# Optimization experiments

Hardware: AMD Instinct MI355X
Metric: run time of the kernel (lower is better)

The kernel has to match this reference:

```python
import jax, jax.numpy as jnp
import numpy as np

D_MODEL = 768
NUM_HEADS = 12
D_K = D_MODEL // NUM_HEADS


def setup_inputs() -> dict:
    key = jax.random.key(0)
    ks = jax.random.split(key, 11)
    B, S = 4, 2048
    s = 1.0 / np.sqrt(D_MODEL)
    return {
        "query": jax.random.normal(ks[0], (B, S, D_MODEL), jnp.float32),
        "key": jax.random.normal(ks[1], (B, S, D_MODEL), jnp.float32),
        "value": jax.random.normal(ks[2], (B, S, D_MODEL), jnp.float32),
        "Wq": jax.random.normal(ks[3], (D_MODEL, D_MODEL), jnp.float32) * s,
        "bq": jnp.zeros((D_MODEL,), jnp.float32),
        "Wk": jax.random.normal(ks[4], (D_MODEL, D_MODEL), jnp.float32) * s,
        "bk": jnp.zeros((D_MODEL,), jnp.float32),
        "Wv": jax.random.normal(ks[5], (D_MODEL, D_MODEL), jnp.float32) * s,
        "bv": jnp.zeros((D_MODEL,), jnp.float32),
        "Wo": jax.random.normal(ks[6], (D_MODEL, D_MODEL), jnp.float32) * s,
        "bo": jnp.zeros((D_MODEL,), jnp.float32),
    }


def reference(query, key, value, Wq, bq, Wk, bk, Wv, bv, Wo, bo):
    B, S, _ = query.shape

    def split_heads(x):  # [B,S,D] -> [B,H,S,dk]
        return x.reshape(B, -1, NUM_HEADS, D_K).transpose(0, 2, 1, 3)

    Q = split_heads(query @ Wq + bq)
    K = split_heads(key @ Wk + bk)
    V = split_heads(value @ Wv + bv)

    scale = 1.0 / jnp.sqrt(jnp.asarray(D_K, Q.dtype))
    scores = jnp.einsum("bhqd,bhkd->bhqk", Q, K) * scale  # [B,H,S,S]
    attn_weights = jax.nn.softmax(scores, axis=-1)
    attn_out = jnp.einsum("bhqk,bhkd->bhqd", attn_weights, V)

    out = attn_out.transpose(0, 2, 1, 3).reshape(B, -1, D_MODEL)
    out = out @ Wo + bo
    return (out, attn_weights)
```

## Files before the change

kernel.cpp:

```cpp
#include <hip/hip_runtime.h>


#define D_MODEL 768
#define NH 12
#define DK 64
#define BATCH 4
#define SEQ 2048
#define BS (BATCH * SEQ)
#define HEADS_TOTAL (BATCH * NH)

__global__ __launch_bounds__(256)
void gemm_bias_kernel(const float* __restrict__ A, const float* __restrict__ W,
                      const float* __restrict__ bias, float* __restrict__ C,
                      int M, int N, int K, int remap)
{
    __shared__ float As[16][136];
    __shared__ float Bs[16][136];
    const int t  = threadIdx.x;
    const int tx = t & 15, ty = t >> 4;
    const int m0 = blockIdx.y * 128;
    const int n0 = blockIdx.x * 128;

    float acc[8][8];
#pragma unroll
    for (int i = 0; i < 8; ++i)
#pragma unroll
        for (int j = 0; j < 8; ++j) acc[i][j] = 0.f;

    for (int kt = 0; kt < K; kt += 16) {
#pragma unroll
        for (int i = 0; i < 2; ++i) {
            int L = t + i * 256;
            int m = L >> 2, kq = (L & 3) * 4;
            float4 v = *(const float4*)(A + (size_t)(m0 + m) * K + kt + kq);
            As[kq + 0][m] = v.x; As[kq + 1][m] = v.y;
            As[kq + 2][m] = v.z; As[kq + 3][m] = v.w;
        }
#pragma unroll
        for (int i = 0; i < 2; ++i) {
            int L = t + i * 256;
            int kk = L >> 5, nq = (L & 31) * 4;
            *(float4*)&Bs[kk][nq] = *(const float4*)(W + (size_t)(kt + kk) * N + n0 + nq);
        }
        __syncthreads();
#pragma unroll
        for (int kk = 0; kk < 16; ++kk) {
            float a[8], b[8];
            *(float4*)&a[0] = *(float4*)&As[kk][ty * 8];
            *(float4*)&a[4] = *(float4*)&As[kk][ty * 8 + 4];
            *(float4*)&b[0] = *(float4*)&Bs[kk][tx * 8];
            *(float4*)&b[4] = *(float4*)&Bs[kk][tx * 8 + 4];
#pragma unroll
            for (int i = 0; i < 8; ++i)
#pragma unroll
                for (int j = 0; j < 8; ++j)
                    acc[i][j] += a[i] * b[j];
        }
        __syncthreads();
    }

    float bv[8];
    *(float4*)&bv[0] = *(const float4*)(bias + n0 + tx * 8);
    *(float4*)&bv[4] = *(const float4*)(bias + n0 + tx * 8 + 4);

#pragma unroll
    for (int i = 0; i < 8; ++i) {
        int m = m0 + ty * 8 + i;
        float o[8];
#pragma unroll
        for (int j = 0; j < 8; ++j) o[j] = acc[i][j] + bv[j];
        float* dst;
        if (remap) {
            int n = n0 + tx * 8;
            int b = m >> 11, s = m & 2047, h = n >> 6, d = n & 63;
            dst = C + (((size_t)(b * NH + h)) << 17) + ((size_t)s << 6) + d;
        } else {
            dst = C + (size_t)m * N + n0 + tx * 8;
        }
        *(float4*)dst       = make_float4(o[0], o[1], o[2], o[3]);
        *(float4*)(dst + 4) = make_float4(o[4], o[5], o[6], o[7]);
    }
}

__global__ __launch_bounds__(256)
void qkv_gemm_kernel(const float* __restrict__ Aq, const float* __restrict__ Ak,
                     const float* __restrict__ Av,
                     const float* __restrict__ Wq, const float* __restrict__ Wk,
                     const float* __restrict__ Wv,
                     const float* __restrict__ bq, const float* __restrict__ bk,
                     const float* __restrict__ bv,
                     float* __restrict__ Cq, float* __restrict__ Ck,
                     float* __restrict__ Cv)
{
    const float* A; const float* W; const float* bias; float* C;
    if (blockIdx.z == 0)      { A = Aq; W = Wq; bias = bq; C = Cq; }
    else if (blockIdx.z == 1) { A = Ak; W = Wk; bias = bk; C = Ck; }
    else                      { A = Av; W = Wv; bias = bv; C = Cv; }

    __shared__ float As[16][136];
    __shared__ float Bs[16][136];
    const int t  = threadIdx.x;
    const int tx = t & 15, ty = t >> 4;
    const int m0 = blockIdx.y * 128;
    const int n0 = blockIdx.x * 128;

    float acc[8][8];
#pragma unroll
    for (int i = 0; i < 8; ++i)
#pragma unroll
        for (int j = 0; j < 8; ++j) acc[i][j] = 0.f;

    for (int kt = 0; kt < D_MODEL; kt += 16) {
#pragma unroll
        for (int i = 0; i < 2; ++i) {
            int L = t + i * 256;
            int m = L >> 2, kq = (L & 3) * 4;
            float4 v = *(const float4*)(A + (size_t)(m0 + m) * D_MODEL + kt + kq);
            As[kq + 0][m] = v.x; As[kq + 1][m] = v.y;
            As[kq + 2][m] = v.z; As[kq + 3][m] = v.w;
        }
#pragma unroll
        for (int i = 0; i < 2; ++i) {
            int L = t + i * 256;
            int kk = L >> 5, nq = (L & 31) * 4;
            *(float4*)&Bs[kk][nq] = *(const float4*)(W + (size_t)(kt + kk) * D_MODEL + n0 + nq);
        }
        __syncthreads();
#pragma unroll
        for (int kk = 0; kk < 16; ++kk) {
            float a[8], b[8];
            *(float4*)&a[0] = *(float4*)&As[kk][ty * 8];
            *(float4*)&a[4] = *(float4*)&As[kk][ty * 8 + 4];
            *(float4*)&b[0] = *(float4*)&Bs[kk][tx * 8];
            *(float4*)&b[4] = *(float4*)&Bs[kk][tx * 8 + 4];
#pragma unroll
            for (int i = 0; i < 8; ++i)
#pragma unroll
                for (int j = 0; j < 8; ++j)
                    acc[i][j] += a[i] * b[j];
        }
        __syncthreads();
    }

    float bvv[8];
    *(float4*)&bvv[0] = *(const float4*)(bias + n0 + tx * 8);
    *(float4*)&bvv[4] = *(const float4*)(bias + n0 + tx * 8 + 4);

#pragma unroll
    for (int i = 0; i < 8; ++i) {
        int m = m0 + ty * 8 + i;
        float o[8];
#pragma unroll
        for (int j = 0; j < 8; ++j) o[j] = acc[i][j] + bvv[j];
        int n = n0 + tx * 8;
        int b = m >> 11, s = m & 2047, h = n >> 6, d = n & 63;
        float* dst = C + (((size_t)(b * NH + h)) << 17) + ((size_t)s << 6) + d;
        *(float4*)dst       = make_float4(o[0], o[1], o[2], o[3]);
        *(float4*)(dst + 4) = make_float4(o[4], o[5], o[6], o[7]);
    }
}

__global__ __launch_bounds__(256)
void scores_kernel(const float* __restrict__ Qh, const float* __restrict__ Kh,
                   float* __restrict__ attn, float* __restrict__ rowsum)
{
    __shared__ float Qs[32][132];
    __shared__ float Ks[32][132];
    const int t  = threadIdx.x;
    const int tx = t & 15, ty = t >> 4;
    const int bh = blockIdx.z;
    const int q0 = blockIdx.y * 128;
    const int n0 = blockIdx.x * 128;
    const float* Q  = Qh + ((size_t)bh << 17);
    const float* Kp = Kh + ((size_t)bh << 17);
    float* attnBH   = attn + ((size_t)bh << 22);

    float acc[8][8];
#pragma unroll
    for (int i = 0; i < 8; ++i)
#pragma unroll
        for (int j = 0; j < 8; ++j) acc[i][j] = 0.f;

    for (int kt = 0; kt < DK; kt += 32) {
#pragma unroll
        for (int i = 0; i < 4; ++i) {
            int L = t + i * 256;
            int r = L >> 3, c4 = (L & 7) * 4;
            float4 v = *(const float4*)(Q  + (size_t)(q0 + r) * DK + kt + c4);
            Qs[c4 + 0][r] = v.x; Qs[c4 + 1][r] = v.y;
            Qs[c4 + 2][r] = v.z; Qs[c4 + 3][r] = v.w;
            float4 w = *(const float4*)(Kp + (size_t)(n0 + r) * DK + kt + c4);
            Ks[c4 + 0][r] = w.x; Ks[c4 + 1][r] = w.y;
            Ks[c4 + 2][r] = w.z; Ks[c4 + 3][r] = w.w;
        }
        __syncthreads();
#pragma unroll
        for (int kk = 0; kk < 32; ++kk) {
            float a[8], b[8];
            *(float4*)&a[0] = *(float4*)&Qs[kk][ty * 8];
            *(float4*)&a[4] = *(float4*)&Qs[kk][ty * 8 + 4];
            *(float4*)&b[0] = *(float4*)&Ks[kk][tx * 8];
            *(float4*)&b[4] = *(float4*)&Ks[kk][tx * 8 + 4];
#pragma unroll
            for (int i = 0; i < 8; ++i)
#pragma unroll
                for (int j = 0; j < 8; ++j)
                    acc[i][j] += a[i] * b[j];
        }
        __syncthreads();
    }

    float rs[8];
#pragma unroll
    for (int i = 0; i < 8; ++i) {
        float r = 0.f;
#pragma unroll
        for (int j = 0; j < 8; ++j) {
            float e = __expf(acc[i][j] * 0.125f);
            acc[i][j] = e;
            r += e;
        }
        rs[i] = r;
        float* dst = attnBH + (size_t)(q0 + ty * 8 + i) * SEQ + n0 + tx * 8;
        *(float4*)dst       = make_float4(acc[i][0], acc[i][1], acc[i][2], acc[i][3]);
        *(float4*)(dst + 4) = make_float4(acc[i][4], acc[i][5], acc[i][6], acc[i][7]);
    }
#pragma unroll
    for (int i = 0; i < 8; ++i) {
        float r = rs[i];
        r += __shfl_xor(r, 1, 16);
        r += __shfl_xor(r, 2, 16);
        r += __shfl_xor(r, 4, 16);
        r += __shfl_xor(r, 8, 16);
        if (tx == 0)
            atomicAdd(rowsum + (size_t)bh * SEQ + q0 + ty * 8 + i, r);
    }
}

__global__ __launch_bounds__(256)
void av_kernel(const float* __restrict__ Vh, float* __restrict__ attn,
               const float* __restrict__ rowsum, float* __restrict__ AO)
{
    __shared__ float es[64][36];
    __shared__ float Vs[32][68];
    __shared__ float rsl[64];
    const int t  = threadIdx.x;
    const int tx = t & 15, ty = t >> 4;
    const int bh = blockIdx.y;
    const int q0 = blockIdx.x * 64;
    const float* V = Vh + ((size_t)bh << 17);
    float* attnBH  = attn + ((size_t)bh << 22);

    if (t < 64) rsl[t] = 1.0f / rowsum[(size_t)bh * SEQ + q0 + t];

    const int er = t >> 3,  ec = (t & 7) * 4;
    const int vr = t >> 4,  vc = (t & 15) * 4;

    float* gA0 = attnBH + (size_t)(q0 + er) * SEQ + ec;
    float* gA1 = attnBH + (size_t)(q0 + er + 32) * SEQ + ec;
    const float* gV0 = V + (size_t)vr * DK + vc;
    const float* gV1 = gV0 + 16 * DK;

    float4 pe0 = *(const float4*)gA0;
    float4 pe1 = *(const float4*)gA1;
    float4 pv0 = *(const float4*)gV0;
    float4 pv1 = *(const float4*)gV1;

    float acc[4][4];
#pragma unroll
    for (int i = 0; i < 4; ++i)
#pragma unroll
        for (int j = 0; j < 4; ++j) acc[i][j] = 0.f;

    __syncthreads();
    const float rinv0 = rsl[er], rinv1 = rsl[er + 32];

    for (int kt = 0; kt < SEQ; kt += 32) {
        *(float4*)&es[er][ec]      = pe0;
        *(float4*)&es[er + 32][ec] = pe1;
        *(float4*)&Vs[vr][vc]      = pv0;
        *(float4*)&Vs[vr + 16][vc] = pv1;
        __syncthreads();

        *(float4*)(gA0 + kt) = make_float4(pe0.x * rinv0, pe0.y * rinv0,
                                           pe0.z * rinv0, pe0.w * rinv0);
        *(float4*)(gA1 + kt) = make_float4(pe1.x * rinv1, pe1.y * rinv1,
                                           pe1.z * rinv1, pe1.w * rinv1);
        if (kt + 32 < SEQ) {
            pe0 = *(const float4*)(gA0 + kt + 32);
            pe1 = *(const float4*)(gA1 + kt + 32);
            pv0 = *(const float4*)(gV0 + (size_t)(kt + 32) * DK);
            pv1 = *(const float4*)(gV1 + (size_t)(kt + 32) * DK);
        }

#pragma unroll
        for (int kk = 0; kk < 32; kk += 4) {
            float4 b0 = *(float4*)&Vs[kk + 0][tx * 4];
            float4 b1 = *(float4*)&Vs[kk + 1][tx * 4];
            float4 b2 = *(float4*)&Vs[kk + 2][tx * 4];
            float4 b3 = *(float4*)&Vs[kk + 3][tx * 4];
#pragma unroll
            for (int i = 0; i < 4; ++i) {
                float4 e = *(float4*)&es[ty * 4 + i][kk];
                acc[i][0] += e.x * b0.x + e.y * b1.x + e.z * b2.x + e.w * b3.x;
                acc[i][1] += e.x * b0.y + e.y * b1.y + e.z * b2.y + e.w * b3.y;
                acc[i][2] += e.x * b0.z + e.y * b1.z + e.z * b2.z + e.w * b3.z;
                acc[i][3] += e.x * b0.w + e.y * b1.w + e.z * b2.w + e.w * b3.w;
            }
        }
        __syncthreads();
    }

    const int b = bh / NH, h = bh % NH;
#pragma unroll
    for (int i = 0; i < 4; ++i) {
        const int q = q0 + ty * 4 + i;
        const float rr = rsl[ty * 4 + i];
        float4 o = make_float4(acc[i][0] * rr, acc[i][1] * rr,
                               acc[i][2] * rr, acc[i][3] * rr);
        *(float4*)(AO + (size_t)(b * SEQ + q) * D_MODEL + h * DK + tx * 4) = o;
    }
}

extern "C" void kernel_launch(void* const* d_in, const int* in_sizes, int n_in,
                              void* d_out, int out_size, void* d_ws, size_t ws_size,
                              hipStream_t stream)
{
    const float* q   = (const float*)d_in[0];
    const float* k   = (const float*)d_in[1];
    const float* v   = (const float*)d_in[2];
    const float* Wq  = (const float*)d_in[3];
    const float* bq  = (const float*)d_in[4];
    const float* Wk  = (const float*)d_in[5];
    const float* bk  = (const float*)d_in[6];
    const float* Wv  = (const float*)d_in[7];
    const float* bv  = (const float*)d_in[8];
    const float* Wo  = (const float*)d_in[9];
    const float* bo  = (const float*)d_in[10];

    float* out  = (float*)d_out;
    float* attn = out + (size_t)BS * D_MODEL;

    const size_t HSZ = (size_t)HEADS_TOTAL * SEQ * DK;
    float* ws     = (float*)d_ws;
    float* Qh     = ws;
    float* Kh     = ws + HSZ;
    float* Vh     = ws + 2 * HSZ;
    float* AO     = ws + 3 * HSZ;
    float* rowsum = ws + 4 * HSZ;

    hipMemsetAsync(rowsum, 0, (size_t)HEADS_TOTAL * SEQ * sizeof(float), stream);

    dim3 gQKV(D_MODEL / 128, BS / 128, 3);
    qkv_gemm_kernel<<<gQKV, 256, 0, stream>>>(q, k, v, Wq, Wk, Wv,
                                              bq, bk, bv, Qh, Kh, Vh);

    scores_kernel<<<dim3(SEQ / 128, SEQ / 128, HEADS_TOTAL), 256, 0, stream>>>(Qh, Kh, attn, rowsum);
    av_kernel<<<dim3(SEQ / 64, HEADS_TOTAL), 256, 0, stream>>>(Vh, attn, rowsum, AO);

    gemm_bias_kernel<<<dim3(D_MODEL / 128, BS / 128), 256, 0, stream>>>(AO, Wo, bo, out, BS, D_MODEL, D_MODEL, 0);
}
```

Baseline: 2.023 ms.

## Retile AV kernel to 128 rows with 8x8 microtiles and swizzled smem; prefetch out GEMM

The attention-times-V kernel now processes 128 query rows per block with 128 threads, each computing an 8x8 output microtile, and uses an XOR swizzle on the shared tile of unnormalized weights. This raises arithmetic intensity and halves how often each V tile is reloaded. The output projection gets a dedicated 64x128-tile GEMM with register prefetch of the next K slice, replacing the generic 128x128 kernel so the grid has more blocks. The trade-offs are more registers per thread and fewer threads per block in the AV kernel, which could lower occupancy.

```diff
diff --git a/kernel.cpp b/kernel.cpp
--- a/kernel.cpp
+++ b/kernel.cpp
@@ -8,79 +8,6 @@
 #define SEQ 2048
 #define BS (BATCH * SEQ)
 #define HEADS_TOTAL (BATCH * NH)
-
-__global__ __launch_bounds__(256)
-void gemm_bias_kernel(const float* __restrict__ A, const float* __restrict__ W,
-                      const float* __restrict__ bias, float* __restrict__ C,
-                      int M, int N, int K, int remap)
-{
-    __shared__ float As[16][136];
-    __shared__ float Bs[16][136];
-    const int t  = threadIdx.x;
-    const int tx = t & 15, ty = t >> 4;
-    const int m0 = blockIdx.y * 128;
-    const int n0 = blockIdx.x * 128;
-
-    float acc[8][8];
-#pragma unroll
-    for (int i = 0; i < 8; ++i)
-#pragma unroll
-        for (int j = 0; j < 8; ++j) acc[i][j] = 0.f;
-
-    for (int kt = 0; kt < K; kt += 16) {
-#pragma unroll
-        for (int i = 0; i < 2; ++i) {
-            int L = t + i * 256;
-            int m = L >> 2, kq = (L & 3) * 4;
-            float4 v = *(const float4*)(A + (size_t)(m0 + m) * K + kt + kq);
-            As[kq + 0][m] = v.x; As[kq + 1][m] = v.y;
-            As[kq + 2][m] = v.z; As[kq + 3][m] = v.w;
-        }
-#pragma unroll
-        for (int i = 0; i < 2; ++i) {
-            int L = t + i * 256;
-            int kk = L >> 5, nq = (L & 31) * 4;
-            *(float4*)&Bs[kk][nq] = *(const float4*)(W + (size_t)(kt + kk) * N + n0 + nq);
-        }
-        __syncthreads();
-#pragma unroll
-        for (int kk = 0; kk < 16; ++kk) {
-            float a[8], b[8];
-            *(float4*)&a[0] = *(float4*)&As[kk][ty * 8];
-            *(float4*)&a[4] = *(float4*)&As[kk][ty * 8 + 4];
-            *(float4*)&b[0] = *(float4*)&Bs[kk][tx * 8];
-            *(float4*)&b[4] = *(float4*)&Bs[kk][tx * 8 + 4];
-#pragma unroll
-            for (int i = 0; i < 8; ++i)
-#pragma unroll
-                for (int j = 0; j < 8; ++j)
-                    acc[i][j] += a[i] * b[j];
-        }
-        __syncthreads();
-    }
-
-    float bv[8];
-    *(float4*)&bv[0] = *(const float4*)(bias + n0 + tx * 8);
-    *(float4*)&bv[4] = *(const float4*)(bias + n0 + tx * 8 + 4);
-
-#pragma unroll
-    for (int i = 0; i < 8; ++i) {
-        int m = m0 + ty * 8 + i;
-        float o[8];
-#pragma unroll
-        for (int j = 0; j < 8; ++j) o[j] = acc[i][j] + bv[j];
-        float* dst;
-        if (remap) {
-            int n = n0 + tx * 8;
-            int b = m >> 11, s = m & 2047, h = n >> 6, d = n & 63;
-            dst = C + (((size_t)(b * NH + h)) << 17) + ((size_t)s << 6) + d;
-        } else {
-            dst = C + (size_t)m * N + n0 + tx * 8;
-        }
-        *(float4*)dst       = make_float4(o[0], o[1], o[2], o[3]);
-        *(float4*)(dst + 4) = make_float4(o[4], o[5], o[6], o[7]);
-    }
-}
 
 __global__ __launch_bounds__(256)
 void qkv_gemm_kernel(const float* __restrict__ Aq, const float* __restrict__ Ak,
@@ -237,88 +164,175 @@
     }
 }
 
-__global__ __launch_bounds__(256)
+#define AV_SWZ(r, c) ((c) ^ ((((r) >> 3) & 7) << 2))
+
+__global__ __launch_bounds__(128)
 void av_kernel(const float* __restrict__ Vh, float* __restrict__ attn,
                const float* __restrict__ rowsum, float* __restrict__ AO)
 {
-    __shared__ float es[64][36];
-    __shared__ float Vs[32][68];
-    __shared__ float rsl[64];
+    __shared__ float es[128][36];
+    __shared__ float Vs[32][72];
+    __shared__ float rsl[128];
+    const int t  = threadIdx.x;
+    const int tx = t & 7;
+    const int ty = t >> 3;
+    const int bh = blockIdx.y;
+    const int q0 = blockIdx.x * 128;
+    const float* V = Vh + ((size_t)bh << 17);
+    float* attnBH  = attn + ((size_t)bh << 22);
+
+    rsl[t] = 1.0f / rowsum[(size_t)bh * SEQ + q0 + t];
+
+    const int er0 = t >> 3;
+    const int ec  = (t & 7) * 4;
+    const int vr0 = t >> 4;
+    const int vc  = (t & 15) * 4;
+
+    float* pA       = attnBH + (size_t)(q0 + er0) * SEQ + ec;
+    const float* pV = V + (size_t)vr0 * DK + vc;
+
+    float4 pe[8], pv[4];
+#pragma unroll
+    for (int i = 0; i < 8; ++i) pe[i] = *(const float4*)(pA + (size_t)i * 16 * SEQ);
+#pragma unroll
+    for (int i = 0; i < 4; ++i) pv[i] = *(const float4*)(pV + (size_t)(8 * i) * DK);
+
+    float acc[8][8] = {};
+
+    __syncthreads();
+    float rinv_st[8];
+#pragma unroll
+    for (int i = 0; i < 8; ++i) rinv_st[i] = rsl[er0 + 16 * i];
+
+    for (int kt = 0; kt < SEQ; kt += 32) {
+#pragma unroll
+        for (int i = 0; i < 8; ++i) {
+            int r = er0 + 16 * i;
+            *(float4*)&es[r][AV_SWZ(r, ec)] = pe[i];
+        }
+#pragma unroll
+        for (int i = 0; i < 4; ++i)
+            *(float4*)&Vs[vr0 + 8 * i][vc] = pv[i];
+        __syncthreads();
+
+#pragma unroll
+        for (int i = 0; i < 8; ++i) {
+            float r = rinv_st[i];
+            *(float4*)(pA + (size_t)i * 16 * SEQ + kt) =
+                make_float4(pe[i].x * r, pe[i].y * r, pe[i].z * r, pe[i].w * r);
+        }
+        if (kt + 32 < SEQ) {
+#pragma unroll
+            for (int i = 0; i < 8; ++i)
+                pe[i] = *(const float4*)(pA + (size_t)i * 16 * SEQ + kt + 32);
+#pragma unroll
+            for (int i = 0; i < 4; ++i)
+                pv[i] = *(const float4*)(pV + (size_t)(kt + 32 + 8 * i) * DK);
+        }
+
+#pragma unroll
+        for (int kk = 0; kk < 32; kk += 4) {
+            float vb[4][8];
+#pragma unroll
+            for (int kb = 0; kb < 4; ++kb) {
+                float4 v0 = *(float4*)&Vs[kk + kb][tx * 8];
+                float4 v1 = *(float4*)&Vs[kk + kb][tx * 8 + 4];
+                vb[kb][0] = v0.x; vb[kb][1] = v0.y; vb[kb][2] = v0.z; vb[kb][3] = v0.w;
+                vb[kb][4] = v1.x; vb[kb][5] = v1.y; vb[kb][6] = v1.z; vb[kb][7] = v1.w;
+            }
+#pragma unroll
+            for (int i = 0; i < 8; ++i) {
+                int r = ty * 8 + i;
+                float4 e = *(float4*)&es[r][AV_SWZ(r, kk)];
+                float ev[4] = {e.x, e.y, e.z, e.w};
+#pragma unroll
+                for (int kb = 0; kb < 4; ++kb)
+#pragma unroll
+                    for (int j = 0; j < 8; ++j)
+                        acc[i][j] += ev[kb] * vb[kb][j];
+            }
+        }
+        __syncthreads();
+    }
+
+    const int b = bh / NH, h = bh % NH;
+#pragma unroll
+    for (int i = 0; i < 8; ++i) {
+        const int q = q0 + ty * 8 + i;
+        const float rr = rsl[ty * 8 + i];
+        float* dst = AO + (size_t)(b * SEQ + q) * D_MODEL + h * DK + tx * 8;
+        *(float4*)dst = make_float4(acc[i][0] * rr, acc[i][1] * rr,
+                                    acc[i][2] * rr, acc[i][3] * rr);
+        *(float4*)(dst + 4) = make_float4(acc[i][4] * rr, acc[i][5] * rr,
+                                          acc[i][6] * rr, acc[i][7] * rr);
+    }
+}
+
+__global__ __launch_bounds__(256)
+void out_gemm_kernel(const float* __restrict__ A, const float* __restrict__ W,
+                     const float* __restrict__ bias, float* __restrict__ C)
+{
+    __shared__ float As[16][68];
+    __shared__ float Bs[16][136];
     const int t  = threadIdx.x;
     const int tx = t & 15, ty = t >> 4;
-    const int bh = blockIdx.y;
-    const int q0 = blockIdx.x * 64;
-    const float* V = Vh + ((size_t)bh << 17);
-    float* attnBH  = attn + ((size_t)bh << 22);
-
-    if (t < 64) rsl[t] = 1.0f / rowsum[(size_t)bh * SEQ + q0 + t];
-
-    const int er = t >> 3,  ec = (t & 7) * 4;
-    const int vr = t >> 4,  vc = (t & 15) * 4;
-
-    float* gA0 = attnBH + (size_t)(q0 + er) * SEQ + ec;
-    float* gA1 = attnBH + (size_t)(q0 + er + 32) * SEQ + ec;
-    const float* gV0 = V + (size_t)vr * DK + vc;
-    const float* gV1 = gV0 + 16 * DK;
-
-    float4 pe0 = *(const float4*)gA0;
-    float4 pe1 = *(const float4*)gA1;
-    float4 pv0 = *(const float4*)gV0;
-    float4 pv1 = *(const float4*)gV1;
-
-    float acc[4][4];
-#pragma unroll
-    for (int i = 0; i < 4; ++i)
-#pragma unroll
-        for (int j = 0; j < 4; ++j) acc[i][j] = 0.f;
-
-    __syncthreads();
-    const float rinv0 = rsl[er], rinv1 = rsl[er + 32];
-
-    for (int kt = 0; kt < SEQ; kt += 32) {
-        *(float4*)&es[er][ec]      = pe0;
-        *(float4*)&es[er + 32][ec] = pe1;
-        *(float4*)&Vs[vr][vc]      = pv0;
-        *(float4*)&Vs[vr + 16][vc] = pv1;
-        __syncthreads();
-
-        *(float4*)(gA0 + kt) = make_float4(pe0.x * rinv0, pe0.y * rinv0,
-                                           pe0.z * rinv0, pe0.w * rinv0);
-        *(float4*)(gA1 + kt) = make_float4(pe1.x * rinv1, pe1.y * rinv1,
-                                           pe1.z * rinv1, pe1.w * rinv1);
-        if (kt + 32 < SEQ) {
-            pe0 = *(const float4*)(gA0 + kt + 32);
-            pe1 = *(const float4*)(gA1 + kt + 32);
-            pv0 = *(const float4*)(gV0 + (size_t)(kt + 32) * DK);
-            pv1 = *(const float4*)(gV1 + (size_t)(kt + 32) * DK);
-        }
-
-#pragma unroll
-        for (int kk = 0; kk < 32; kk += 4) {
-            float4 b0 = *(float4*)&Vs[kk + 0][tx * 4];
-            float4 b1 = *(float4*)&Vs[kk + 1][tx * 4];
-            float4 b2 = *(float4*)&Vs[kk + 2][tx * 4];
-            float4 b3 = *(float4*)&Vs[kk + 3][tx * 4];
-#pragma unroll
-            for (int i = 0; i < 4; ++i) {
-                float4 e = *(float4*)&es[ty * 4 + i][kk];
-                acc[i][0] += e.x * b0.x + e.y * b1.x + e.z * b2.x + e.w * b3.x;
-                acc[i][1] += e.x * b0.y + e.y * b1.y + e.z * b2.y + e.w * b3.y;
-                acc[i][2] += e.x * b0.z + e.y * b1.z + e.z * b2.z + e.w * b3.z;
-                acc[i][3] += e.x * b0.w + e.y * b1.w + e.z * b2.w + e.w * b3.w;
-            }
-        }
-        __syncthreads();
-    }
-
-    const int b = bh / NH, h = bh % NH;
+    const int m0 = blockIdx.y * 64;
+    const int n0 = blockIdx.x * 128;
+
+    const int am = t >> 2, akq = (t & 3) * 4;
+    const int bk0 = t >> 5,         bn0 = (t & 31) * 4;
+    const int bk1 = (t + 256) >> 5, bn1 = bn0;
+
+    const float* pA = A + (size_t)(m0 + am) * D_MODEL + akq;
+    const float* pB = W + n0;
+
+    float4 pa  = *(const float4*)pA;
+    float4 pb0 = *(const float4*)(pB + (size_t)bk0 * D_MODEL + bn0);
+    float4 pb1 = *(const float4*)(pB + (size_t)bk1 * D_MODEL + bn1);
+
+    float acc[4][8] = {};
+
+    for (int kt = 0; kt < D_MODEL; kt += 16) {
+        As[akq + 0][am] = pa.x; As[akq + 1][am] = pa.y;
+        As[akq + 2][am] = pa.z; As[akq + 3][am] = pa.w;
+        *(float4*)&Bs[bk0][bn0] = pb0;
+        *(float4*)&Bs[bk1][bn1] = pb1;
+        __syncthreads();
+
+        if (kt + 16 < D_MODEL) {
+            pa  = *(const float4*)(pA + kt + 16);
+            pb0 = *(const float4*)(pB + (size_t)(kt + 16 + bk0) * D_MODEL + bn0);
+            pb1 = *(const float4*)(pB + (size_t)(kt + 16 + bk1) * D_MODEL + bn1);
+        }
+
+#pragma unroll
+        for (int kk = 0; kk < 16; ++kk) {
+            float4 a = *(float4*)&As[kk][ty * 4];
+            float b[8];
+            *(float4*)&b[0] = *(float4*)&Bs[kk][tx * 8];
+            *(float4*)&b[4] = *(float4*)&Bs[kk][tx * 8 + 4];
+            float av[4] = {a.x, a.y, a.z, a.w};
+#pragma unroll
+            for (int i = 0; i < 4; ++i)
+#pragma unroll
+                for (int j = 0; j < 8; ++j)
+                    acc[i][j] += av[i] * b[j];
+        }
+        __syncthreads();
+    }
+
+    float bv[8];
+    *(float4*)&bv[0] = *(const float4*)(bias + n0 + tx * 8);
+    *(float4*)&bv[4] = *(const float4*)(bias + n0 + tx * 8 + 4);
+
 #pragma unroll
     for (int i = 0; i < 4; ++i) {
-        const int q = q0 + ty * 4 + i;
-        const float rr = rsl[ty * 4 + i];
-        float4 o = make_float4(acc[i][0] * rr, acc[i][1] * rr,
-                               acc[i][2] * rr, acc[i][3] * rr);
-        *(float4*)(AO + (size_t)(b * SEQ + q) * D_MODEL + h * DK + tx * 4) = o;
+        int m = m0 + ty * 4 + i;
+        float* dst = C + (size_t)m * D_MODEL + n0 + tx * 8;
+        *(float4*)dst       = make_float4(acc[i][0] + bv[0], acc[i][1] + bv[1],
+                                          acc[i][2] + bv[2], acc[i][3] + bv[3]);
+        *(float4*)(dst + 4) = make_float4(acc[i][4] + bv[4], acc[i][5] + bv[5],
+                                          acc[i][6] + bv[6], acc[i][7] + bv[7]);
     }
 }
 
@@ -356,7 +370,8 @@
                                               bq, bk, bv, Qh, Kh, Vh);
 
     scores_kernel<<<dim3(SEQ / 128, SEQ / 128, HEADS_TOTAL), 256, 0, stream>>>(Qh, Kh, attn, rowsum);
-    av_kernel<<<dim3(SEQ / 64, HEADS_TOTAL), 256, 0, stream>>>(Vh, attn, rowsum, AO);
-
-    gemm_bias_kernel<<<dim3(D_MODEL / 128, BS / 128), 256, 0, stream>>>(AO, Wo, bo, out, BS, D_MODEL, D_MODEL, 0);
-}
+
+    av_kernel<<<dim3(SEQ / 128, HEADS_TOTAL), 128, 0, stream>>>(Vh, attn, rowsum, AO);
+
+    out_gemm_kernel<<<dim3(D_MODEL / 128, BS / 64), 256, 0, stream>>>(AO, Wo, bo, out);
+}
```

Measured after the change: 2.243 ms. 1.11x slower.
